# Kernel tuning notes

Measured on AMD Instinct MI355X. Metric: run time of the kernel, lower is better.

The kernel has to match this reference:

```python
import jax, jax.numpy as jnp
import numpy as np

B, N, D_IN, D_OUT = 8, 2048, 256, 256
BN_EPS = 1e-5
SELU_ALPHA = 1.6732632423543772
SELU_SCALE = 1.0507009873554805


def setup_inputs() -> dict:
    key = jax.random.key(0)
    k1, k2, k3, k4 = jax.random.split(key, 4)
    lim_lin = 1.0 / np.sqrt(D_IN)
    return {
        "x": jax.random.normal(k1, (B, N, D_IN), dtype=jnp.float32),
        "w_map": jax.random.uniform(k2, (D_IN,), jnp.float32, -lim_lin, lim_lin),
        "w_att": jax.random.uniform(k3, (D_OUT, D_IN), jnp.float32, -lim_lin, lim_lin),
        "w_res": jax.random.uniform(k4, (D_OUT, D_IN), jnp.float32, -lim_lin, lim_lin),
        "gamma": jnp.ones((D_OUT,), jnp.float32),
        "beta": jnp.zeros((D_OUT,), jnp.float32),
    }


def _selu(x):
    x_clamped = jnp.clip(x, -10.0, 10.0)
    return SELU_SCALE * jnp.where(x > 0, x, SELU_ALPHA * (jnp.exp(x_clamped) - 1.0))


def reference(x, w_map, w_att, w_res, gamma, beta):
    # scores[b,i,j] = sum_d w_map[d] * x[b,i,d] * x[b,j,d]  (== W_map(x_i*x_j))
    scores = jnp.einsum("bid,bjd->bij", x * w_map, x)  # [B,N,N]
    attn = jax.nn.softmax(scores, axis=-1)
    aggregated = jnp.einsum("bij,bjd->bid", attn, x)  # [B,N,D]
    out = aggregated @ w_att.T + x @ w_res.T  # [B,N,D_OUT]
    # BatchNorm1d in training mode: stats over (batch, nodes) per channel, biased var
    mean = jnp.mean(out, axis=(0, 1))
    var = jnp.mean(jnp.square(out - mean), axis=(0, 1))
    out = (out - mean) * jax.lax.rsqrt(var + BN_EPS) * gamma + beta
    return _selu(out)
```

## Files before the change

### kernel.cpp

```cpp
#include <hip/hip_runtime.h>
#include <hip/hip_bf16.h>


typedef __attribute__((ext_vector_type(8))) short  bf16x8;
typedef __attribute__((ext_vector_type(4))) float  f32x4;

#define MFMA16(a, b, c) __builtin_amdgcn_mfma_f32_16x16x32_bf16((a), (b), (c), 0, 0, 0)

constexpr int   NB = 8, NN = 2048, ND = 256;
constexpr int   ROWS = NB * NN;
constexpr float BN_EPS = 1e-5f;
constexpr float SELU_ALPHA = 1.6732632423543772f;
constexpr float SELU_SCALE = 1.0507009873554805f;

__device__ __forceinline__ unsigned short f2bf(float f) {
  union { float f; unsigned int u; } v; v.f = f;
  unsigned int u = v.u;
  u += 0x7FFFu + ((u >> 16) & 1u);
  return (unsigned short)(u >> 16);
}
__device__ __forceinline__ float bf2f(unsigned short h) {
  union { float f; unsigned int u; } v; v.u = ((unsigned int)h) << 16;
  return v.f;
}

__device__ __forceinline__ void async_copy16(const unsigned short* g, unsigned short* l) {
  __builtin_amdgcn_global_load_lds(
      (const __attribute__((address_space(1))) void*)g,
      (__attribute__((address_space(3))) void*)l, 16, 0, 0);
}

__global__ __launch_bounds__(256) void k0_prep(const float* __restrict__ x,
                                               const float* __restrict__ w_att,
                                               const float* __restrict__ w_res,
                                               unsigned short* __restrict__ AX,
                                               unsigned short* __restrict__ Xt,
                                               unsigned short* __restrict__ WC,
                                               float* __restrict__ sums) {
  __shared__ unsigned short Ls[64 * 264];
  const int t = threadIdx.x;
  if (blockIdx.x >= 256) {
    const int bid = blockIdx.x - 256;
    if (bid == 0 && t < 128)
      ((float4*)sums)[t] = make_float4(0.f, 0.f, 0.f, 0.f);
    int f = (bid * 256 + t) * 8;
    int c = f >> 9, k = f & 511;
    const float* src = (k < 256) ? (w_att + c * 256 + k) : (w_res + c * 256 + (k - 256));
    float4 a = *(const float4*)src;
    float4 b = *(const float4*)(src + 4);
    union { unsigned short s[8]; uint4 v; } o;
    o.s[0] = f2bf(a.x); o.s[1] = f2bf(a.y); o.s[2] = f2bf(a.z); o.s[3] = f2bf(a.w);
    o.s[4] = f2bf(b.x); o.s[5] = f2bf(b.y); o.s[6] = f2bf(b.z); o.s[7] = f2bf(b.w);
    *(uint4*)(WC + f) = o.v;
    return;
  }
  const int b = blockIdx.x & 7, rt = blockIdx.x >> 3;
  const int grb = b * NN + rt * 64;
  const int c = (t & 31) * 8, r0 = t >> 5;
#pragma unroll
  for (int q = 0; q < 8; ++q) {
    int r = r0 + q * 8;
    const float* xp = x + (size_t)(grb + r) * 256 + c;
    float4 a = *(const float4*)xp;
    float4 d = *(const float4*)(xp + 4);
    union { unsigned short s[8]; uint4 v; } xb;
    xb.s[0] = f2bf(a.x); xb.s[1] = f2bf(a.y); xb.s[2] = f2bf(a.z); xb.s[3] = f2bf(a.w);
    xb.s[4] = f2bf(d.x); xb.s[5] = f2bf(d.y); xb.s[6] = f2bf(d.z); xb.s[7] = f2bf(d.w);
    *(uint4*)(AX + (size_t)(grb + r) * 512 + 256 + c) = xb.v;
    *(uint4*)&Ls[r * 264 + c] = xb.v;
  }
  __syncthreads();
  unsigned short* dst = Xt + ((size_t)b * 256 + t) * 2048 + rt * 64;
#pragma unroll
  for (int k = 0; k < 8; ++k) {
    union { unsigned short s[8]; uint4 v; } o;
#pragma unroll
    for (int j = 0; j < 8; ++j) o.s[j] = Ls[(k * 8 + j) * 264 + t];
    *(uint4*)(dst + k * 8) = o.v;
  }
}

__global__ __launch_bounds__(512, 2) void k1_attn(const float* __restrict__ w_map,
                                                  const unsigned short* AX,
                                                  const unsigned short* __restrict__ Xt,
                                                  unsigned short* AXw) {
  __shared__ unsigned short Ks[2][2][32 * 256];
  __shared__ unsigned short Vt[2][2][256 * 32];
  __shared__ unsigned short Psw[8][16 * 40];

  const int t = threadIdx.x;
  const int w = t >> 6, lane = t & 63, l15 = lane & 15, quad = lane >> 4;
  const int g = w >> 2, wg = w & 3;
  const int b = blockIdx.x & 7, it = blockIdx.x >> 3;
  const int gib = b * NN + it * 64;
  const unsigned short* Xtb = Xt + (size_t)b * 256 * 2048;
  const unsigned short* AXr = AX + (size_t)b * NN * 512 + 256;
  const int jgbase = g * 1024;

  int ksOff[4], vtOff[4];
#pragma unroll
  for (int q = 0; q < 4; ++q) {
    int j = wg * 8 + q * 2 + (lane >> 5);
    int ck = (lane & 31) ^ (j & 7);
    ksOff[q] = j * 512 + ck * 8;
    int d = wg * 64 + q * 16 + (lane >> 2);
    int cv = (lane & 3) ^ ((d >> 1) & 3);
    vtOff[q] = d * 2048 + cv * 8;
  }
  const int ldsOff = wg * 2048 + lane * 8;

  bf16x8 qf[8];
  {
    const unsigned short* xrow = AXr + (size_t)(it * 64 + wg * 16 + l15) * 512;
#pragma unroll
    for (int kc = 0; kc < 8; ++kc) {
      bf16x8 xb = *(const bf16x8*)(xrow + kc * 32 + quad * 8);
      const float* wp = w_map + kc * 32 + quad * 8;
      float4 w0 = *(const float4*)wp, w1 = *(const float4*)(wp + 4);
      float wv[8] = {w0.x, w0.y, w0.z, w0.w, w1.x, w1.y, w1.z, w1.w};
      bf16x8 q;
#pragma unroll
      for (int i = 0; i < 8; ++i)
        q[i] = (short)f2bf(bf2f((unsigned short)xb[i]) * wv[i]);
      qf[kc] = q;
    }
  }

  const f32x4 fz = {0.f, 0.f, 0.f, 0.f};
  f32x4 oacc[16];
#pragma unroll
  for (int i = 0; i < 16; ++i) oacc[i] = fz;
  f32x4 oL = fz;

  bf16x8 onesFrag;
  {
    short o1 = (l15 == 0) ? (short)0x3F80 : (short)0;
#pragma unroll
    for (int i = 0; i < 8; ++i) onesFrag[i] = o1;
  }

#pragma unroll
  for (int q = 0; q < 4; ++q)
    async_copy16(AXr + (size_t)jgbase * 512 + ksOff[q], &Ks[g][0][ldsOff + q * 512]);
#pragma unroll
  for (int q = 0; q < 4; ++q)
    async_copy16(Xtb + jgbase + vtOff[q], &Vt[g][0][ldsOff + q * 512]);

  for (int jt = 0; jt < 32; ++jt) {
    const int cur = jt & 1;
    __syncthreads();
    if (jt < 31) {
      const int jb1 = jgbase + (jt + 1) * 32;
#pragma unroll
      for (int q = 0; q < 4; ++q)
        async_copy16(AXr + (size_t)jb1 * 512 + ksOff[q], &Ks[g][cur ^ 1][ldsOff + q * 512]);
#pragma unroll
      for (int q = 0; q < 4; ++q)
        async_copy16(Xtb + jb1 + vtOff[q], &Vt[g][cur ^ 1][ldsOff + q * 512]);
    }
#pragma unroll
    for (int jm = 0; jm < 2; ++jm) {
      const int j = jm * 16 + l15;
      f32x4 s = fz;
#pragma unroll
      for (int kc = 0; kc < 8; ++kc) {
        int ckk = kc * 4 + quad;
        bf16x8 kf = *(const bf16x8*)&Ks[g][cur][j * 256 + ((ckk ^ (j & 7)) * 8)];
        s = MFMA16(kf, qf[kc], s);
      }
      ushort4 pk;
      pk.x = f2bf(__expf(s[0])); pk.y = f2bf(__expf(s[1]));
      pk.z = f2bf(__expf(s[2])); pk.w = f2bf(__expf(s[3]));
      *(ushort4*)&Psw[w][l15 * 40 + jm * 16 + quad * 4] = pk;
    }
    bf16x8 af = *(const bf16x8*)&Psw[w][l15 * 40 + quad * 8];
#pragma unroll
    for (int nti = 0; nti < 16; ++nti) {
      const int d = nti * 16 + l15;
      bf16x8 vf = *(const bf16x8*)&Vt[g][cur][d * 32 + ((quad ^ ((d >> 1) & 3)) * 8)];
      oacc[nti] = MFMA16(af, vf, oacc[nti]);
    }
    oL = MFMA16(af, onesFrag, oL);
  }

  __syncthreads();
  float* Obuf = (float*)&Ks[0][0][0];
  float* Lb   = (float*)&Vt[0][0][0];
  if (g == 1) {
#pragma unroll
    for (int nti = 0; nti < 16; ++nti)
#pragma unroll
      for (int r = 0; r < 4; ++r) {
        int row = quad * 4 + r;
        Obuf[wg * 4096 + row * 256 + (((nti + quad) & 15) << 4) + l15] = oacc[nti][r];
      }
    if (l15 == 0) {
#pragma unroll
      for (int r = 0; r < 4; ++r) Lb[wg * 16 + quad * 4 + r] = oL[r];
    }
  }
  __syncthreads();
  if (g == 0) {
    float ls[4];
#pragma unroll
    for (int r = 0; r < 4; ++r) ls[r] = Lb[wg * 16 + quad * 4 + r];
#pragma unroll
    for (int nti = 0; nti < 16; ++nti)
#pragma unroll
      for (int r = 0; r < 4; ++r) {
        int row = quad * 4 + r;
        oacc[nti][r] += Obuf[wg * 4096 + row * 256 + (((nti + quad) & 15) << 4) + l15];
      }
    float li[4];
#pragma unroll
    for (int r = 0; r < 4; ++r)
      li[r] = 1.0f / (__shfl(oL[r], lane & 48) + ls[r]);
#pragma unroll
    for (int nti = 0; nti < 16; ++nti) {
      const int gcol = nti * 16 + l15;
#pragma unroll
      for (int r = 0; r < 4; ++r) {
        const int grow = gib + wg * 16 + quad * 4 + r;
        AXw[(size_t)grow * 512 + gcol] = f2bf(oacc[nti][r] * li[r]);
      }
    }
  }
}

__global__ __launch_bounds__(256, 2) void k2_gemm(const unsigned short* __restrict__ AX,
                                                  const unsigned short* __restrict__ WC,
                                                  float* __restrict__ out,
                                                  float* __restrict__ sums) {
  __shared__ unsigned short As[2][128 * 64];
  __shared__ unsigned short Bs[2][64 * 64];
  __shared__ float cs[64], cq[64];
  const int t = threadIdx.x;
  const int w = t >> 6, lane = t & 63, l15 = lane & 15, quad = lane >> 4;
  const int m0 = (blockIdx.x >> 2) * 128, n0 = (blockIdx.x & 3) * 64;
  if (t < 64) { cs[t] = 0.f; cq[t] = 0.f; }

  int aOff[4], bOff[2];
#pragma unroll
  for (int q = 0; q < 4; ++q) {
    int u = t + q * 256, row = u >> 3, c = (u & 7) ^ (row & 7);
    aOff[q] = (m0 + row) * 512 + c * 8;
  }
#pragma unroll
  for (int q = 0; q < 2; ++q) {
    int u = t + q * 256, row = u >> 3, c = (u & 7) ^ (row & 7);
    bOff[q] = (n0 + row) * 512 + c * 8;
  }
  const int ldsA = t * 8;
  const int ldsB = t * 8;

  const f32x4 fz = {0.f, 0.f, 0.f, 0.f};
  f32x4 acc[4][2];
#pragma unroll
  for (int i = 0; i < 4; ++i) { acc[i][0] = fz; acc[i][1] = fz; }

#pragma unroll
  for (int q = 0; q < 4; ++q)
    async_copy16(AX + (size_t)aOff[q], &As[0][ldsA + q * 2048]);
#pragma unroll
  for (int q = 0; q < 2; ++q)
    async_copy16(WC + (size_t)bOff[q], &Bs[0][ldsB + q * 2048]);

  for (int ki = 0; ki < 8; ++ki) {
    const int cur = ki & 1;
    __syncthreads();
    if (ki < 7) {
      const int kk = (ki + 1) * 64;
#pragma unroll
      for (int q = 0; q < 4; ++q)
        async_copy16(AX + (size_t)(aOff[q] + kk), &As[cur ^ 1][ldsA + q * 2048]);
#pragma unroll
      for (int q = 0; q < 2; ++q)
        async_copy16(WC + (size_t)(bOff[q] + kk), &Bs[cur ^ 1][ldsB + q * 2048]);
    }
#pragma unroll
    for (int kc = 0; kc < 2; ++kc) {
      const int c = kc * 4 + quad;
      const int rb0 = (w >> 1) * 32 + l15, rb1 = rb0 + 16;
      bf16x8 b0 = *(const bf16x8*)&Bs[cur][rb0 * 64 + ((c ^ (rb0 & 7)) * 8)];
      bf16x8 b1 = *(const bf16x8*)&Bs[cur][rb1 * 64 + ((c ^ (rb1 & 7)) * 8)];
#pragma unroll
      for (int mt = 0; mt < 4; ++mt) {
        const int ra = (w & 1) * 64 + mt * 16 + l15;
        bf16x8 af = *(const bf16x8*)&As[cur][ra * 64 + ((c ^ (ra & 7)) * 8)];
        acc[mt][0] = MFMA16(af, b0, acc[mt][0]);
        acc[mt][1] = MFMA16(af, b1, acc[mt][1]);
      }
    }
  }
#pragma unroll
  for (int mt = 0; mt < 4; ++mt)
#pragma unroll
    for (int nt = 0; nt < 2; ++nt)
#pragma unroll
      for (int r = 0; r < 4; ++r) {
        int grow = m0 + (w & 1) * 64 + mt * 16 + quad * 4 + r;
        int gcol = n0 + (w >> 1) * 32 + nt * 16 + l15;
        out[(size_t)grow * 256 + gcol] = acc[mt][nt][r];
      }
#pragma unroll
  for (int nt = 0; nt < 2; ++nt) {
    float a = 0.f, b2 = 0.f;
#pragma unroll
    for (int mt = 0; mt < 4; ++mt)
#pragma unroll
      for (int r = 0; r < 4; ++r) {
        float v = acc[mt][nt][r];
        a += v; b2 += v * v;
      }
    a += __shfl_xor(a, 16);  a += __shfl_xor(a, 32);
    b2 += __shfl_xor(b2, 16); b2 += __shfl_xor(b2, 32);
    if (quad == 0) {
      int ci = (w >> 1) * 32 + nt * 16 + l15;
      atomicAdd(&cs[ci], a);
      atomicAdd(&cq[ci], b2);
    }
  }
  __syncthreads();
  if (t < 64) {
    atomicAdd(&sums[n0 + t], cs[t]);
    atomicAdd(&sums[256 + n0 + t], cq[t]);
  }
}

__global__ __launch_bounds__(256) void k4_bn_selu(float* __restrict__ out,
                                                  const float* __restrict__ sums,
                                                  const float* __restrict__ gamma,
                                                  const float* __restrict__ beta) {
  __shared__ float sc[256], sh[256];
  const int t = threadIdx.x;
  {
    const float inv_m = 1.0f / 16384.0f;
    float mean = sums[t] * inv_m;
    float var = sums[256 + t] * inv_m - mean * mean;
    float s = rsqrtf(var + BN_EPS) * gamma[t];
    sc[t] = s;
    sh[t] = beta[t] - mean * s;
  }
  __syncthreads();
  int f = (blockIdx.x * 256 + t) * 8;
  int c = f & 255;
  float4 v0 = *(const float4*)(out + f);
  float4 v1 = *(const float4*)(out + f + 4);
  float vv[8] = {v0.x, v0.y, v0.z, v0.w, v1.x, v1.y, v1.z, v1.w};
#pragma unroll
  for (int k = 0; k < 8; ++k) {
    int ch = c + k;
    float y = vv[k] * sc[ch] + sh[ch];
    float yc = fminf(fmaxf(y, -10.f), 10.f);
    float r = (y > 0.f) ? y : (SELU_ALPHA * (expf(yc) - 1.0f));
    vv[k] = SELU_SCALE * r;
  }
  float4 o0 = {vv[0], vv[1], vv[2], vv[3]};
  float4 o1 = {vv[4], vv[5], vv[6], vv[7]};
  *(float4*)(out + f) = o0;
  *(float4*)(out + f + 4) = o1;
}

extern "C" void kernel_launch(void* const* d_in, const int* in_sizes, int n_in,
                              void* d_out, int out_size, void* d_ws, size_t ws_size,
                              hipStream_t stream) {
  const float* x     = (const float*)d_in[0];
  const float* w_map = (const float*)d_in[1];
  const float* w_att = (const float*)d_in[2];
  const float* w_res = (const float*)d_in[3];
  const float* gamma = (const float*)d_in[4];
  const float* beta  = (const float*)d_in[5];
  float* out = (float*)d_out;

  unsigned short* AX = (unsigned short*)d_ws;
  unsigned short* Xt = AX + (size_t)ROWS * 512;
  unsigned short* WC = Xt + (size_t)NB * 256 * 2048;
  float* sums = (float*)(WC + 256 * 512);

  k0_prep<<<320, 256, 0, stream>>>(x, w_att, w_res, AX, Xt, WC, sums);
  k1_attn<<<256, 512, 0, stream>>>(w_map, AX, Xt, AX);
  k2_gemm<<<512, 256, 0, stream>>>(AX, WC, out, sums);
  k4_bn_selu<<<2048, 256, 0, stream>>>(out, sums, gamma, beta);
}
```

Measured before the change: 163.0 us.

## Fuse BatchNorm+SELU into GEMM via grid barrier; halve prep tile rows

Removes the separate BN/SELU kernel. The GEMM now waits at a global atomic-counter barrier until all 512 blocks have added their channel statistics, then applies the normalization and SELU to its accumulators in registers and writes the final output once. This drops a full read and write of the fp32 output and one kernel launch. The barrier needs all 512 blocks to be resident at the same time (launch bounds 256 threads, 2 blocks per CU), and the counter is zeroed in the prep kernel. Separately, the prep kernel handles 32-row tiles instead of 64, so it launches twice as many blocks.

```diff
diff --git a/kernel.cpp b/kernel.cpp
--- a/kernel.cpp
+++ b/kernel.cpp
@@ -37,11 +37,11 @@
                                                unsigned short* __restrict__ Xt,
                                                unsigned short* __restrict__ WC,
                                                float* __restrict__ sums) {
-  __shared__ unsigned short Ls[64 * 264];
+  __shared__ unsigned short Ls[32 * 264];
   const int t = threadIdx.x;
-  if (blockIdx.x >= 256) {
-    const int bid = blockIdx.x - 256;
-    if (bid == 0 && t < 128)
+  if (blockIdx.x >= 512) {
+    const int bid = blockIdx.x - 512;
+    if (bid == 0 && t < 130)
       ((float4*)sums)[t] = make_float4(0.f, 0.f, 0.f, 0.f);
     int f = (bid * 256 + t) * 8;
     int c = f >> 9, k = f & 511;
@@ -55,10 +55,10 @@
     return;
   }
   const int b = blockIdx.x & 7, rt = blockIdx.x >> 3;
-  const int grb = b * NN + rt * 64;
+  const int grb = b * NN + rt * 32;
   const int c = (t & 31) * 8, r0 = t >> 5;
 #pragma unroll
-  for (int q = 0; q < 8; ++q) {
+  for (int q = 0; q < 4; ++q) {
     int r = r0 + q * 8;
     const float* xp = x + (size_t)(grb + r) * 256 + c;
     float4 a = *(const float4*)xp;
@@ -70,9 +70,9 @@
     *(uint4*)&Ls[r * 264 + c] = xb.v;
   }
   __syncthreads();
-  unsigned short* dst = Xt + ((size_t)b * 256 + t) * 2048 + rt * 64;
-#pragma unroll
-  for (int k = 0; k < 8; ++k) {
+  unsigned short* dst = Xt + ((size_t)b * 256 + t) * 2048 + rt * 32;
+#pragma unroll
+  for (int k = 0; k < 4; ++k) {
     union { unsigned short s[8]; uint4 v; } o;
 #pragma unroll
     for (int j = 0; j < 8; ++j) o.s[j] = Ls[(k * 8 + j) * 264 + t];
@@ -230,7 +230,9 @@
 __global__ __launch_bounds__(256, 2) void k2_gemm(const unsigned short* __restrict__ AX,
                                                   const unsigned short* __restrict__ WC,
                                                   float* __restrict__ out,
-                                                  float* __restrict__ sums) {
+                                                  float* __restrict__ sums,
+                                                  const float* __restrict__ gamma,
+                                                  const float* __restrict__ beta) {
   __shared__ unsigned short As[2][128 * 64];
   __shared__ unsigned short Bs[2][64 * 64];
   __shared__ float cs[64], cq[64];
@@ -250,8 +252,7 @@
     int u = t + q * 256, row = u >> 3, c = (u & 7) ^ (row & 7);
     bOff[q] = (n0 + row) * 512 + c * 8;
   }
-  const int ldsA = t * 8;
-  const int ldsB = t * 8;
+  const int ldsA = t * 8, ldsB = t * 8;
 
   const f32x4 fz = {0.f, 0.f, 0.f, 0.f};
   f32x4 acc[4][2];
@@ -292,16 +293,6 @@
       }
     }
   }
-#pragma unroll
-  for (int mt = 0; mt < 4; ++mt)
-#pragma unroll
-    for (int nt = 0; nt < 2; ++nt)
-#pragma unroll
-      for (int r = 0; r < 4; ++r) {
-        int grow = m0 + (w & 1) * 64 + mt * 16 + quad * 4 + r;
-        int gcol = n0 + (w >> 1) * 32 + nt * 16 + l15;
-        out[(size_t)grow * 256 + gcol] = acc[mt][nt][r];
-      }
 #pragma unroll
   for (int nt = 0; nt < 2; ++nt) {
     float a = 0.f, b2 = 0.f;
@@ -325,40 +316,40 @@
     atomicAdd(&sums[n0 + t], cs[t]);
     atomicAdd(&sums[256 + n0 + t], cq[t]);
   }
-}
-
-__global__ __launch_bounds__(256) void k4_bn_selu(float* __restrict__ out,
-                                                  const float* __restrict__ sums,
-                                                  const float* __restrict__ gamma,
-                                                  const float* __restrict__ beta) {
-  __shared__ float sc[256], sh[256];
-  const int t = threadIdx.x;
-  {
+  unsigned int* cnt = (unsigned int*)(sums + 512);
+  __threadfence();
+  __syncthreads();
+  if (t == 0) {
+    atomicAdd(cnt, 1u);
+    while (atomicAdd(cnt, 0u) < 512u) __builtin_amdgcn_s_sleep(8);
+  }
+  __syncthreads();
+  if (t < 64) {
     const float inv_m = 1.0f / 16384.0f;
-    float mean = sums[t] * inv_m;
-    float var = sums[256 + t] * inv_m - mean * mean;
-    float s = rsqrtf(var + BN_EPS) * gamma[t];
-    sc[t] = s;
-    sh[t] = beta[t] - mean * s;
-  }
-  __syncthreads();
-  int f = (blockIdx.x * 256 + t) * 8;
-  int c = f & 255;
-  float4 v0 = *(const float4*)(out + f);
-  float4 v1 = *(const float4*)(out + f + 4);
-  float vv[8] = {v0.x, v0.y, v0.z, v0.w, v1.x, v1.y, v1.z, v1.w};
-#pragma unroll
-  for (int k = 0; k < 8; ++k) {
-    int ch = c + k;
-    float y = vv[k] * sc[ch] + sh[ch];
-    float yc = fminf(fmaxf(y, -10.f), 10.f);
-    float r = (y > 0.f) ? y : (SELU_ALPHA * (expf(yc) - 1.0f));
-    vv[k] = SELU_SCALE * r;
-  }
-  float4 o0 = {vv[0], vv[1], vv[2], vv[3]};
-  float4 o1 = {vv[4], vv[5], vv[6], vv[7]};
-  *(float4*)(out + f) = o0;
-  *(float4*)(out + f + 4) = o1;
+    float s1 = atomicAdd(&sums[n0 + t], 0.f) * inv_m;
+    float s2 = atomicAdd(&sums[256 + n0 + t], 0.f) * inv_m;
+    float var = s2 - s1 * s1;
+    float sc = rsqrtf(var + BN_EPS) * gamma[n0 + t];
+    cs[t] = sc;
+    cq[t] = beta[n0 + t] - s1 * sc;
+  }
+  __syncthreads();
+#pragma unroll
+  for (int nt = 0; nt < 2; ++nt) {
+    const int ci = (w >> 1) * 32 + nt * 16 + l15;
+    const float sc = cs[ci], sh = cq[ci];
+    const int gcol = n0 + ci;
+#pragma unroll
+    for (int mt = 0; mt < 4; ++mt)
+#pragma unroll
+      for (int r = 0; r < 4; ++r) {
+        int grow = m0 + (w & 1) * 64 + mt * 16 + quad * 4 + r;
+        float y = acc[mt][nt][r] * sc + sh;
+        float yc = fminf(fmaxf(y, -10.f), 10.f);
+        float rr = (y > 0.f) ? y : (SELU_ALPHA * (expf(yc) - 1.0f));
+        out[(size_t)grow * 256 + gcol] = SELU_SCALE * rr;
+      }
+  }
 }
 
 extern "C" void kernel_launch(void* const* d_in, const int* in_sizes, int n_in,
@@ -377,8 +368,7 @@
   unsigned short* WC = Xt + (size_t)NB * 256 * 2048;
   float* sums = (float*)(WC + 256 * 512);
 
-  k0_prep<<<320, 256, 0, stream>>>(x, w_att, w_res, AX, Xt, WC, sums);
+  k0_prep<<<576, 256, 0, stream>>>(x, w_att, w_res, AX, Xt, WC, sums);
   k1_attn<<<256, 512, 0, stream>>>(w_map, AX, Xt, AX);
-  k2_gemm<<<512, 256, 0, stream>>>(AX, WC, out, sums);
-  k4_bn_selu<<<2048, 256, 0, stream>>>(out, sums, gamma, beta);
-}
+  k2_gemm<<<512, 256, 0, stream>>>(AX, WC, out, sums, gamma, beta);
+}
```

Result: slower. 202.8 us (+24.4%).

## Fuse output projection GEMM into attention kernel epilogue

Applied to the files above, without the earlier changes.

The attention kernel now keeps the normalized aggregated rows in LDS and multiplies them directly against the concatenated [w_att|w_res] weights, together with the bf16 x rows, to produce the output and the BatchNorm partial sums. This removes the separate GEMM kernel launch and the global round trip of the aggregated bf16 activations. The prep kernel writes a compact 256-wide x buffer and uses 32-row tiles across more blocks. Risks: the epilogue reads its weight and x fragments straight from global memory without LDS staging, only 256 blocks do the projection work, and the per-column atomics to global sums increase.

```diff
diff --git a/kernel.cpp b/kernel.cpp
--- a/kernel.cpp
+++ b/kernel.cpp
@@ -33,14 +33,14 @@
 __global__ __launch_bounds__(256) void k0_prep(const float* __restrict__ x,
                                                const float* __restrict__ w_att,
                                                const float* __restrict__ w_res,
-                                               unsigned short* __restrict__ AX,
+                                               unsigned short* __restrict__ Xr,
                                                unsigned short* __restrict__ Xt,
                                                unsigned short* __restrict__ WC,
                                                float* __restrict__ sums) {
-  __shared__ unsigned short Ls[64 * 264];
+  __shared__ unsigned short Ls[32 * 264];
   const int t = threadIdx.x;
-  if (blockIdx.x >= 256) {
-    const int bid = blockIdx.x - 256;
+  if (blockIdx.x >= 512) {
+    const int bid = blockIdx.x - 512;
     if (bid == 0 && t < 128)
       ((float4*)sums)[t] = make_float4(0.f, 0.f, 0.f, 0.f);
     int f = (bid * 256 + t) * 8;
@@ -55,10 +55,10 @@
     return;
   }
   const int b = blockIdx.x & 7, rt = blockIdx.x >> 3;
-  const int grb = b * NN + rt * 64;
+  const int grb = b * NN + rt * 32;
   const int c = (t & 31) * 8, r0 = t >> 5;
 #pragma unroll
-  for (int q = 0; q < 8; ++q) {
+  for (int q = 0; q < 4; ++q) {
     int r = r0 + q * 8;
     const float* xp = x + (size_t)(grb + r) * 256 + c;
     float4 a = *(const float4*)xp;
@@ -66,13 +66,13 @@
     union { unsigned short s[8]; uint4 v; } xb;
     xb.s[0] = f2bf(a.x); xb.s[1] = f2bf(a.y); xb.s[2] = f2bf(a.z); xb.s[3] = f2bf(a.w);
     xb.s[4] = f2bf(d.x); xb.s[5] = f2bf(d.y); xb.s[6] = f2bf(d.z); xb.s[7] = f2bf(d.w);
-    *(uint4*)(AX + (size_t)(grb + r) * 512 + 256 + c) = xb.v;
+    *(uint4*)(Xr + (size_t)(grb + r) * 256 + c) = xb.v;
     *(uint4*)&Ls[r * 264 + c] = xb.v;
   }
   __syncthreads();
-  unsigned short* dst = Xt + ((size_t)b * 256 + t) * 2048 + rt * 64;
-#pragma unroll
-  for (int k = 0; k < 8; ++k) {
+  unsigned short* dst = Xt + ((size_t)b * 256 + t) * 2048 + rt * 32;
+#pragma unroll
+  for (int k = 0; k < 4; ++k) {
     union { unsigned short s[8]; uint4 v; } o;
 #pragma unroll
     for (int j = 0; j < 8; ++j) o.s[j] = Ls[(k * 8 + j) * 264 + t];
@@ -81,12 +81,15 @@
 }
 
 __global__ __launch_bounds__(512, 2) void k1_attn(const float* __restrict__ w_map,
-                                                  const unsigned short* AX,
+                                                  const unsigned short* __restrict__ Xr,
                                                   const unsigned short* __restrict__ Xt,
-                                                  unsigned short* AXw) {
+                                                  const unsigned short* __restrict__ WC,
+                                                  float* __restrict__ out,
+                                                  float* __restrict__ sums) {
   __shared__ unsigned short Ks[2][2][32 * 256];
   __shared__ unsigned short Vt[2][2][256 * 32];
   __shared__ unsigned short Psw[8][16 * 40];
+  __shared__ float Lb[64];
 
   const int t = threadIdx.x;
   const int w = t >> 6, lane = t & 63, l15 = lane & 15, quad = lane >> 4;
@@ -94,7 +97,7 @@
   const int b = blockIdx.x & 7, it = blockIdx.x >> 3;
   const int gib = b * NN + it * 64;
   const unsigned short* Xtb = Xt + (size_t)b * 256 * 2048;
-  const unsigned short* AXr = AX + (size_t)b * NN * 512 + 256;
+  const unsigned short* Xrb = Xr + (size_t)b * NN * 256;
   const int jgbase = g * 1024;
 
   int ksOff[4], vtOff[4];
@@ -102,7 +105,7 @@
   for (int q = 0; q < 4; ++q) {
     int j = wg * 8 + q * 2 + (lane >> 5);
     int ck = (lane & 31) ^ (j & 7);
-    ksOff[q] = j * 512 + ck * 8;
+    ksOff[q] = j * 256 + ck * 8;
     int d = wg * 64 + q * 16 + (lane >> 2);
     int cv = (lane & 3) ^ ((d >> 1) & 3);
     vtOff[q] = d * 2048 + cv * 8;
@@ -111,7 +114,7 @@
 
   bf16x8 qf[8];
   {
-    const unsigned short* xrow = AXr + (size_t)(it * 64 + wg * 16 + l15) * 512;
+    const unsigned short* xrow = Xrb + (size_t)(it * 64 + wg * 16 + l15) * 256;
 #pragma unroll
     for (int kc = 0; kc < 8; ++kc) {
       bf16x8 xb = *(const bf16x8*)(xrow + kc * 32 + quad * 8);
@@ -141,7 +144,7 @@
 
 #pragma unroll
   for (int q = 0; q < 4; ++q)
-    async_copy16(AXr + (size_t)jgbase * 512 + ksOff[q], &Ks[g][0][ldsOff + q * 512]);
+    async_copy16(Xrb + (size_t)jgbase * 256 + ksOff[q], &Ks[g][0][ldsOff + q * 512]);
 #pragma unroll
   for (int q = 0; q < 4; ++q)
     async_copy16(Xtb + jgbase + vtOff[q], &Vt[g][0][ldsOff + q * 512]);
@@ -153,7 +156,7 @@
       const int jb1 = jgbase + (jt + 1) * 32;
 #pragma unroll
       for (int q = 0; q < 4; ++q)
-        async_copy16(AXr + (size_t)jb1 * 512 + ksOff[q], &Ks[g][cur ^ 1][ldsOff + q * 512]);
+        async_copy16(Xrb + (size_t)jb1 * 256 + ksOff[q], &Ks[g][cur ^ 1][ldsOff + q * 512]);
 #pragma unroll
       for (int q = 0; q < 4; ++q)
         async_copy16(Xtb + jb1 + vtOff[q], &Vt[g][cur ^ 1][ldsOff + q * 512]);
@@ -185,7 +188,7 @@
 
   __syncthreads();
   float* Obuf = (float*)&Ks[0][0][0];
-  float* Lb   = (float*)&Vt[0][0][0];
+  unsigned short* Agg = &Vt[0][0][0];
   if (g == 1) {
 #pragma unroll
     for (int nti = 0; nti < 16; ++nti)
@@ -216,114 +219,64 @@
     for (int r = 0; r < 4; ++r)
       li[r] = 1.0f / (__shfl(oL[r], lane & 48) + ls[r]);
 #pragma unroll
-    for (int nti = 0; nti < 16; ++nti) {
-      const int gcol = nti * 16 + l15;
-#pragma unroll
-      for (int r = 0; r < 4; ++r) {
-        const int grow = gib + wg * 16 + quad * 4 + r;
-        AXw[(size_t)grow * 512 + gcol] = f2bf(oacc[nti][r] * li[r]);
-      }
-    }
-  }
-}
-
-__global__ __launch_bounds__(256, 2) void k2_gemm(const unsigned short* __restrict__ AX,
-                                                  const unsigned short* __restrict__ WC,
-                                                  float* __restrict__ out,
-                                                  float* __restrict__ sums) {
-  __shared__ unsigned short As[2][128 * 64];
-  __shared__ unsigned short Bs[2][64 * 64];
-  __shared__ float cs[64], cq[64];
-  const int t = threadIdx.x;
-  const int w = t >> 6, lane = t & 63, l15 = lane & 15, quad = lane >> 4;
-  const int m0 = (blockIdx.x >> 2) * 128, n0 = (blockIdx.x & 3) * 64;
-  if (t < 64) { cs[t] = 0.f; cq[t] = 0.f; }
-
-  int aOff[4], bOff[2];
-#pragma unroll
-  for (int q = 0; q < 4; ++q) {
-    int u = t + q * 256, row = u >> 3, c = (u & 7) ^ (row & 7);
-    aOff[q] = (m0 + row) * 512 + c * 8;
-  }
-#pragma unroll
-  for (int q = 0; q < 2; ++q) {
-    int u = t + q * 256, row = u >> 3, c = (u & 7) ^ (row & 7);
-    bOff[q] = (n0 + row) * 512 + c * 8;
-  }
-  const int ldsA = t * 8;
-  const int ldsB = t * 8;
-
-  const f32x4 fz = {0.f, 0.f, 0.f, 0.f};
-  f32x4 acc[4][2];
-#pragma unroll
-  for (int i = 0; i < 4; ++i) { acc[i][0] = fz; acc[i][1] = fz; }
-
-#pragma unroll
-  for (int q = 0; q < 4; ++q)
-    async_copy16(AX + (size_t)aOff[q], &As[0][ldsA + q * 2048]);
-#pragma unroll
-  for (int q = 0; q < 2; ++q)
-    async_copy16(WC + (size_t)bOff[q], &Bs[0][ldsB + q * 2048]);
-
-  for (int ki = 0; ki < 8; ++ki) {
-    const int cur = ki & 1;
-    __syncthreads();
-    if (ki < 7) {
-      const int kk = (ki + 1) * 64;
-#pragma unroll
-      for (int q = 0; q < 4; ++q)
-        async_copy16(AX + (size_t)(aOff[q] + kk), &As[cur ^ 1][ldsA + q * 2048]);
-#pragma unroll
-      for (int q = 0; q < 2; ++q)
-        async_copy16(WC + (size_t)(bOff[q] + kk), &Bs[cur ^ 1][ldsB + q * 2048]);
-    }
-#pragma unroll
-    for (int kc = 0; kc < 2; ++kc) {
-      const int c = kc * 4 + quad;
-      const int rb0 = (w >> 1) * 32 + l15, rb1 = rb0 + 16;
-      bf16x8 b0 = *(const bf16x8*)&Bs[cur][rb0 * 64 + ((c ^ (rb0 & 7)) * 8)];
-      bf16x8 b1 = *(const bf16x8*)&Bs[cur][rb1 * 64 + ((c ^ (rb1 & 7)) * 8)];
-#pragma unroll
-      for (int mt = 0; mt < 4; ++mt) {
-        const int ra = (w & 1) * 64 + mt * 16 + l15;
-        bf16x8 af = *(const bf16x8*)&As[cur][ra * 64 + ((c ^ (ra & 7)) * 8)];
-        acc[mt][0] = MFMA16(af, b0, acc[mt][0]);
-        acc[mt][1] = MFMA16(af, b1, acc[mt][1]);
-      }
-    }
-  }
-#pragma unroll
-  for (int mt = 0; mt < 4; ++mt)
-#pragma unroll
-    for (int nt = 0; nt < 2; ++nt)
-#pragma unroll
-      for (int r = 0; r < 4; ++r) {
-        int grow = m0 + (w & 1) * 64 + mt * 16 + quad * 4 + r;
-        int gcol = n0 + (w >> 1) * 32 + nt * 16 + l15;
-        out[(size_t)grow * 256 + gcol] = acc[mt][nt][r];
-      }
+    for (int nti = 0; nti < 16; ++nti)
+#pragma unroll
+      for (int r = 0; r < 4; ++r)
+        Agg[(wg * 16 + quad * 4 + r) * 264 + nti * 16 + l15] =
+            f2bf(oacc[nti][r] * li[r]);
+  }
+  __syncthreads();
+
+  f32x4 eacc[2][4];
+#pragma unroll
+  for (int i = 0; i < 2; ++i)
+#pragma unroll
+    for (int j = 0; j < 4; ++j) eacc[i][j] = fz;
+
+#pragma unroll
+  for (int kc = 0; kc < 16; ++kc) {
+    bf16x8 bf0 = *(const bf16x8*)(WC + (size_t)(w * 32 + l15) * 512 + kc * 32 + quad * 8);
+    bf16x8 bf1 = *(const bf16x8*)(WC + (size_t)(w * 32 + 16 + l15) * 512 + kc * 32 + quad * 8);
+#pragma unroll
+    for (int rt = 0; rt < 4; ++rt) {
+      bf16x8 af;
+      if (kc < 8)
+        af = *(const bf16x8*)&Agg[(rt * 16 + l15) * 264 + kc * 32 + quad * 8];
+      else
+        af = *(const bf16x8*)(Xrb + (size_t)(it * 64 + rt * 16 + l15) * 256 +
+                              (kc - 8) * 32 + quad * 8);
+      eacc[0][rt] = MFMA16(af, bf0, eacc[0][rt]);
+      eacc[1][rt] = MFMA16(af, bf1, eacc[1][rt]);
+    }
+  }
 #pragma unroll
   for (int nt = 0; nt < 2; ++nt) {
     float a = 0.f, b2 = 0.f;
 #pragma unroll
-    for (int mt = 0; mt < 4; ++mt)
+    for (int rt = 0; rt < 4; ++rt)
 #pragma unroll
       for (int r = 0; r < 4; ++r) {
-        float v = acc[mt][nt][r];
+        float v = eacc[nt][rt][r];
         a += v; b2 += v * v;
       }
     a += __shfl_xor(a, 16);  a += __shfl_xor(a, 32);
     b2 += __shfl_xor(b2, 16); b2 += __shfl_xor(b2, 32);
     if (quad == 0) {
-      int ci = (w >> 1) * 32 + nt * 16 + l15;
-      atomicAdd(&cs[ci], a);
-      atomicAdd(&cq[ci], b2);
-    }
-  }
-  __syncthreads();
-  if (t < 64) {
-    atomicAdd(&sums[n0 + t], cs[t]);
-    atomicAdd(&sums[256 + n0 + t], cq[t]);
+      int ci = w * 32 + nt * 16 + l15;
+      atomicAdd(&sums[ci], a);
+      atomicAdd(&sums[256 + ci], b2);
+    }
+  }
+#pragma unroll
+  for (int nt = 0; nt < 2; ++nt) {
+    const int gcol = w * 32 + nt * 16 + l15;
+#pragma unroll
+    for (int rt = 0; rt < 4; ++rt)
+#pragma unroll
+      for (int r = 0; r < 4; ++r) {
+        const int grow = gib + rt * 16 + quad * 4 + r;
+        out[(size_t)grow * 256 + gcol] = eacc[nt][rt][r];
+      }
   }
 }
 
@@ -372,13 +325,12 @@
   const float* beta  = (const float*)d_in[5];
   float* out = (float*)d_out;
 
-  unsigned short* AX = (unsigned short*)d_ws;
-  unsigned short* Xt = AX + (size_t)ROWS * 512;
+  unsigned short* Xr = (unsigned short*)d_ws;
+  unsigned short* Xt = Xr + (size_t)ROWS * 256;
   unsigned short* WC = Xt + (size_t)NB * 256 * 2048;
   float* sums = (float*)(WC + 256 * 512);
 
-  k0_prep<<<320, 256, 0, stream>>>(x, w_att, w_res, AX, Xt, WC, sums);
-  k1_attn<<<256, 512, 0, stream>>>(w_map, AX, Xt, AX);
-  k2_gemm<<<512, 256, 0, stream>>>(AX, WC, out, sums);
+  k0_prep<<<576, 256, 0, stream>>>(x, w_att, w_res, Xr, Xt, WC, sums);
+  k1_attn<<<256, 512, 0, stream>>>(w_map, Xr, Xt, WC, out, sums);
   k4_bn_selu<<<2048, 256, 0, stream>>>(out, sums, gamma, beta);
 }
```

Measured after the change: 167.4 us. 1.03x slower.
